# Performance work log

Measured on AMD Instinct MI355X. Metric: run time of the kernel, lower is better.

## Reference

```python
import jax, jax.numpy as jnp
import numpy as np

V = 50000   # input_size == output_size (one-hot vocab)
H = 256     # hidden_size
B = 512     # batch_size
L = 1       # num_layers

def setup_inputs() -> dict:
    key = jax.random.key(0)
    ks = jax.random.split(key, 9)
    s = 1.0 / np.sqrt(H)  # torch default uniform(-1/sqrt(H), 1/sqrt(H))
    inp = {
        "input": jax.random.randint(ks[0], (B,), 0, V, dtype=jnp.int64 if jax.config.jax_enable_x64 else jnp.int32),
        "target": jax.random.randint(ks[1], (B,), 0, V, dtype=jnp.int64 if jax.config.jax_enable_x64 else jnp.int32),
        "hidden": jax.random.normal(ks[2], (L, B, H), dtype=jnp.float32),
        "w_ih": jax.random.uniform(ks[3], (3 * H, V), jnp.float32, -s, s),
        "w_hh": jax.random.uniform(ks[4], (3 * H, H), jnp.float32, -s, s),
        "b_ih": jax.random.uniform(ks[5], (3 * H,), jnp.float32, -s, s),
        "b_hh": jax.random.uniform(ks[6], (3 * H,), jnp.float32, -s, s),
        "w_out": jax.random.uniform(ks[7], (V, H), jnp.float32, -s, s),
        "b_out": jax.random.uniform(ks[8], (V,), jnp.float32, -s, s),
    }
    return inp

def reference(input, target, hidden, w_ih, w_hh, b_ih, b_hh, w_out, b_out):
    # one-hot(input) @ w_ih.T is exactly a row-gather from w_ih.T  -> (B, 3H)
    h0 = hidden[0]                              # (B, H), num_layers == 1
    x_proj = w_ih.T[input] + b_ih               # (B, 3H)
    h_proj = h0 @ w_hh.T + b_hh                 # (B, 3H)
    xr, xz, xn = jnp.split(x_proj, 3, axis=-1)
    hr, hz, hn = jnp.split(h_proj, 3, axis=-1)
    r = jax.nn.sigmoid(xr + hr)                 # reset gate
    z = jax.nn.sigmoid(xz + hz)                 # update gate
    n = jnp.tanh(xn + r * hn)                   # candidate
    h1 = (1.0 - z) * n + z * h0                 # (B, H)
    logit = jnp.tanh(h1 @ w_out.T + b_out)      # (B, V)
    return logit, h1[None]                      # (B,V), (1,B,H)
```

## Files before the change

### kernel.cpp

```cpp
#include <hip/hip_runtime.h>
#include <hip/hip_bf16.h>

#define VOCAB 50000
#define HID   256
#define BATCH 512
#define GH    768

typedef __attribute__((ext_vector_type(8))) __bf16 bf16x8;
typedef __attribute__((ext_vector_type(4))) float f32x4;

union BFrag {
    bf16x8 v;
    uint4  q;
    unsigned short u[8];
};

__device__ __forceinline__ unsigned short f2bf(float f) {
    unsigned int x = __builtin_bit_cast(unsigned int, f);
    x += 0x7FFFu + ((x >> 16) & 1u);
    return (unsigned short)(x >> 16);
}

__device__ __forceinline__ float fast_sigmoid(float x) {
    return 1.0f / (1.0f + __expf(-x));
}
__device__ __forceinline__ float fast_tanh(float x) {
    return 1.0f - 2.0f / (1.0f + __expf(2.0f * x));
}

template <int EPI, int ASRC>
__global__ __launch_bounds__(256) void gemm_nt(
    const void* __restrict__ Asrc, const float* __restrict__ Bm,
    float* __restrict__ C, const float* __restrict__ bias,
    int Ncols, int mChunks)
{
    __shared__ char ldsA[64 * 512];

    const int tid  = threadIdx.x;
    const int wid  = tid >> 6;
    const int lane = tid & 63;
    const int r    = lane & 15;
    const int g    = lane >> 4;
    const int nbase = blockIdx.x * 64;
    const int col   = nbase + wid * 16 + r;
    const int bcol  = col < Ncols ? col : (Ncols - 1);

    BFrag bf[8];
    {
        const float4* wrow = reinterpret_cast<const float4*>(Bm + (size_t)bcol * 256);
        #pragma unroll
        for (int kk = 0; kk < 8; kk++) {
            float4 lo = wrow[kk * 8 + g * 2];
            float4 hi = wrow[kk * 8 + g * 2 + 1];
            bf[kk].u[0] = f2bf(lo.x); bf[kk].u[1] = f2bf(lo.y);
            bf[kk].u[2] = f2bf(lo.z); bf[kk].u[3] = f2bf(lo.w);
            bf[kk].u[4] = f2bf(hi.x); bf[kk].u[5] = f2bf(hi.y);
            bf[kk].u[6] = f2bf(hi.z); bf[kk].u[7] = f2bf(hi.w);
        }
    }
    float biasv = 0.0f;
    if (EPI == 1) biasv = bias[bcol];

    for (int c = 0; c < mChunks; c++) {
        const int mbase = (blockIdx.y * mChunks + c) * 64;

        if (ASRC == 1) {
            const uint4* src = reinterpret_cast<const uint4*>(
                (const unsigned short*)Asrc + (size_t)mbase * 256);
            #pragma unroll
            for (int i = 0; i < 8; i++) {
                int u   = tid + i * 256;
                int row = u >> 5, c16 = u & 31;
                uint4 vv = src[row * 32 + c16];
                int byte = (row * 512 + c16 * 16) ^ ((row & 7) << 4);
                *reinterpret_cast<uint4*>(&ldsA[byte]) = vv;
            }
        } else {
            const float4* src = reinterpret_cast<const float4*>(
                (const float*)Asrc + (size_t)mbase * 256);
            #pragma unroll
            for (int i = 0; i < 8; i++) {
                int u   = tid + i * 256;
                int row = u >> 5, c16 = u & 31;
                float4 lo = src[row * 64 + c16 * 2];
                float4 hi = src[row * 64 + c16 * 2 + 1];
                BFrag t;
                t.u[0] = f2bf(lo.x); t.u[1] = f2bf(lo.y);
                t.u[2] = f2bf(lo.z); t.u[3] = f2bf(lo.w);
                t.u[4] = f2bf(hi.x); t.u[5] = f2bf(hi.y);
                t.u[6] = f2bf(hi.z); t.u[7] = f2bf(hi.w);
                int byte = (row * 512 + c16 * 16) ^ ((row & 7) << 4);
                *reinterpret_cast<uint4*>(&ldsA[byte]) = t.q;
            }
        }
        __syncthreads();

        f32x4 acc[4];
        #pragma unroll
        for (int m = 0; m < 4; m++) acc[m] = (f32x4){0.f, 0.f, 0.f, 0.f};

        #pragma unroll
        for (int kk = 0; kk < 8; kk++) {
            #pragma unroll
            for (int m = 0; m < 4; m++) {
                int arow = m * 16 + r;
                int byte = (arow * 512 + kk * 64 + g * 16) ^ ((arow & 7) << 4);
                BFrag a;
                a.q = *reinterpret_cast<const uint4*>(&ldsA[byte]);
                acc[m] = __builtin_amdgcn_mfma_f32_16x16x32_bf16(a.v, bf[kk].v, acc[m], 0, 0, 0);
            }
        }

        if (col < Ncols) {
            #pragma unroll
            for (int m = 0; m < 4; m++) {
                #pragma unroll
                for (int j = 0; j < 4; j++) {
                    int row = mbase + m * 16 + g * 4 + j;
                    float v = acc[m][j];
                    if (EPI == 1) v = fast_tanh(v + biasv);
                    C[(size_t)row * Ncols + col] = v;
                }
            }
        }
        __syncthreads();
    }
}

__global__ __launch_bounds__(256) void gru_gate(
    const int* __restrict__ inp, const float* __restrict__ hidden,
    const float* __restrict__ w_ih, const float* __restrict__ b_ih,
    const float* __restrict__ b_hh, const float* __restrict__ hproj,
    float* __restrict__ h1out, unsigned short* __restrict__ h1bf)
{
    const int b = blockIdx.x;
    const int k = threadIdx.x;
    const int c = inp[b];

    float xr = w_ih[(size_t)k * VOCAB + c]         + b_ih[k];
    float xz = w_ih[(size_t)(k + 256) * VOCAB + c] + b_ih[k + 256];
    float xn = w_ih[(size_t)(k + 512) * VOCAB + c] + b_ih[k + 512];

    float hr = hproj[b * GH + k]       + b_hh[k];
    float hz = hproj[b * GH + 256 + k] + b_hh[k + 256];
    float hn = hproj[b * GH + 512 + k] + b_hh[k + 512];

    float rg = fast_sigmoid(xr + hr);
    float zg = fast_sigmoid(xz + hz);
    float ng = fast_tanh(xn + rg * hn);
    float h0 = hidden[b * HID + k];
    float h1 = (1.0f - zg) * ng + zg * h0;

    h1out[b * HID + k] = h1;
    h1bf[b * HID + k]  = f2bf(h1);
}

extern "C" void kernel_launch(void* const* d_in, const int* in_sizes, int n_in,
                              void* d_out, int out_size, void* d_ws, size_t ws_size,
                              hipStream_t stream) {
    const int*   input  = (const int*)  d_in[0];
    const float* hidden = (const float*)d_in[2];
    const float* w_ih   = (const float*)d_in[3];
    const float* w_hh   = (const float*)d_in[4];
    const float* b_ih   = (const float*)d_in[5];
    const float* b_hh   = (const float*)d_in[6];
    const float* w_out  = (const float*)d_in[7];
    const float* b_out  = (const float*)d_in[8];

    float* logit = (float*)d_out;
    float* h1    = (float*)d_out + (size_t)BATCH * VOCAB;

    float*          hproj = (float*)d_ws;
    unsigned short* h1bf  = (unsigned short*)((char*)d_ws + (size_t)BATCH * GH * 4);

    dim3 g1(GH / 64, BATCH / 64);
    gemm_nt<0, 0><<<g1, 256, 0, stream>>>(hidden, w_hh, hproj, nullptr, GH, 1);

    gru_gate<<<BATCH, 256, 0, stream>>>(input, hidden, w_ih, b_ih, b_hh, hproj, h1, h1bf);

    dim3 g3((VOCAB + 63) / 64, 1);
    gemm_nt<1, 1><<<g3, 256, 0, stream>>>(h1bf, w_out, logit, b_out, VOCAB, 8);
}
```

Baseline: 63.18 us.

## Drop LDS staging of A operand; load fragments directly from global with nontemporal access

The GEMM kernel no longer stages the A tile into shared memory behind barriers. Each wave now loads its MFMA A fragments directly from global memory, relying on L2/L1 because the bf16 h1 matrix is small and shared across all blocks. Weight loads for the large output projection and the logit stores use nontemporal hints to avoid polluting cache. The risk is that redundant global loads per wave, with 4x duplication across waves, add latency that LDS reuse previously hid.

```diff
diff --git a/kernel.cpp b/kernel.cpp
--- a/kernel.cpp
+++ b/kernel.cpp
@@ -8,10 +8,11 @@
 
 typedef __attribute__((ext_vector_type(8))) __bf16 bf16x8;
 typedef __attribute__((ext_vector_type(4))) float f32x4;
+typedef __attribute__((ext_vector_type(4))) unsigned int u32x4;
 
 union BFrag {
     bf16x8 v;
-    uint4  q;
+    u32x4  q;
     unsigned short u[8];
 };
 
@@ -28,34 +29,41 @@
     return 1.0f - 2.0f / (1.0f + __expf(2.0f * x));
 }
 
-template <int EPI, int ASRC>
+__device__ __forceinline__ void cvt8(BFrag& t, f32x4 lo, f32x4 hi) {
+    t.u[0] = f2bf(lo.x); t.u[1] = f2bf(lo.y);
+    t.u[2] = f2bf(lo.z); t.u[3] = f2bf(lo.w);
+    t.u[4] = f2bf(hi.x); t.u[5] = f2bf(hi.y);
+    t.u[6] = f2bf(hi.z); t.u[7] = f2bf(hi.w);
+}
+
+template <int EPI, int ASRC, int NTB>
 __global__ __launch_bounds__(256) void gemm_nt(
     const void* __restrict__ Asrc, const float* __restrict__ Bm,
     float* __restrict__ C, const float* __restrict__ bias,
     int Ncols, int mChunks)
 {
-    __shared__ char ldsA[64 * 512];
-
     const int tid  = threadIdx.x;
     const int wid  = tid >> 6;
     const int lane = tid & 63;
     const int r    = lane & 15;
     const int g    = lane >> 4;
-    const int nbase = blockIdx.x * 64;
-    const int col   = nbase + wid * 16 + r;
-    const int bcol  = col < Ncols ? col : (Ncols - 1);
+    const int col  = blockIdx.x * 64 + wid * 16 + r;
+    const int bcol = col < Ncols ? col : (Ncols - 1);
 
     BFrag bf[8];
     {
-        const float4* wrow = reinterpret_cast<const float4*>(Bm + (size_t)bcol * 256);
+        const f32x4* wrow = reinterpret_cast<const f32x4*>(Bm + (size_t)bcol * 256);
         #pragma unroll
         for (int kk = 0; kk < 8; kk++) {
-            float4 lo = wrow[kk * 8 + g * 2];
-            float4 hi = wrow[kk * 8 + g * 2 + 1];
-            bf[kk].u[0] = f2bf(lo.x); bf[kk].u[1] = f2bf(lo.y);
-            bf[kk].u[2] = f2bf(lo.z); bf[kk].u[3] = f2bf(lo.w);
-            bf[kk].u[4] = f2bf(hi.x); bf[kk].u[5] = f2bf(hi.y);
-            bf[kk].u[6] = f2bf(hi.z); bf[kk].u[7] = f2bf(hi.w);
+            f32x4 lo, hi;
+            if (NTB) {
+                lo = __builtin_nontemporal_load(&wrow[kk * 8 + g * 2]);
+                hi = __builtin_nontemporal_load(&wrow[kk * 8 + g * 2 + 1]);
+            } else {
+                lo = wrow[kk * 8 + g * 2];
+                hi = wrow[kk * 8 + g * 2 + 1];
+            }
+            cvt8(bf[kk], lo, hi);
         }
     }
     float biasv = 0.0f;
@@ -63,37 +71,6 @@
 
     for (int c = 0; c < mChunks; c++) {
         const int mbase = (blockIdx.y * mChunks + c) * 64;
-
-        if (ASRC == 1) {
-            const uint4* src = reinterpret_cast<const uint4*>(
-                (const unsigned short*)Asrc + (size_t)mbase * 256);
-            #pragma unroll
-            for (int i = 0; i < 8; i++) {
-                int u   = tid + i * 256;
-                int row = u >> 5, c16 = u & 31;
-                uint4 vv = src[row * 32 + c16];
-                int byte = (row * 512 + c16 * 16) ^ ((row & 7) << 4);
-                *reinterpret_cast<uint4*>(&ldsA[byte]) = vv;
-            }
-        } else {
-            const float4* src = reinterpret_cast<const float4*>(
-                (const float*)Asrc + (size_t)mbase * 256);
-            #pragma unroll
-            for (int i = 0; i < 8; i++) {
-                int u   = tid + i * 256;
-                int row = u >> 5, c16 = u & 31;
-                float4 lo = src[row * 64 + c16 * 2];
-                float4 hi = src[row * 64 + c16 * 2 + 1];
-                BFrag t;
-                t.u[0] = f2bf(lo.x); t.u[1] = f2bf(lo.y);
-                t.u[2] = f2bf(lo.z); t.u[3] = f2bf(lo.w);
-                t.u[4] = f2bf(hi.x); t.u[5] = f2bf(hi.y);
-                t.u[6] = f2bf(hi.z); t.u[7] = f2bf(hi.w);
-                int byte = (row * 512 + c16 * 16) ^ ((row & 7) << 4);
-                *reinterpret_cast<uint4*>(&ldsA[byte]) = t.q;
-            }
-        }
-        __syncthreads();
 
         f32x4 acc[4];
         #pragma unroll
@@ -103,10 +80,17 @@
         for (int kk = 0; kk < 8; kk++) {
             #pragma unroll
             for (int m = 0; m < 4; m++) {
-                int arow = m * 16 + r;
-                int byte = (arow * 512 + kk * 64 + g * 16) ^ ((arow & 7) << 4);
+                const int arow = mbase + m * 16 + r;
                 BFrag a;
-                a.q = *reinterpret_cast<const uint4*>(&ldsA[byte]);
+                if (ASRC == 1) {
+                    const u32x4* ap = reinterpret_cast<const u32x4*>(
+                        (const unsigned short*)Asrc + (size_t)arow * 256);
+                    a.q = ap[kk * 4 + g];
+                } else {
+                    const f32x4* ap = reinterpret_cast<const f32x4*>(
+                        (const float*)Asrc + (size_t)arow * 256);
+                    cvt8(a, ap[kk * 8 + g * 2], ap[kk * 8 + g * 2 + 1]);
+                }
                 acc[m] = __builtin_amdgcn_mfma_f32_16x16x32_bf16(a.v, bf[kk].v, acc[m], 0, 0, 0);
             }
         }
@@ -118,12 +102,15 @@
                 for (int j = 0; j < 4; j++) {
                     int row = mbase + m * 16 + g * 4 + j;
                     float v = acc[m][j];
-                    if (EPI == 1) v = fast_tanh(v + biasv);
-                    C[(size_t)row * Ncols + col] = v;
+                    if (EPI == 1) {
+                        v = fast_tanh(v + biasv);
+                        __builtin_nontemporal_store(v, &C[(size_t)row * Ncols + col]);
+                    } else {
+                        C[(size_t)row * Ncols + col] = v;
+                    }
                 }
             }
         }
-        __syncthreads();
     }
 }
 
@@ -174,10 +161,10 @@
     unsigned short* h1bf  = (unsigned short*)((char*)d_ws + (size_t)BATCH * GH * 4);
 
     dim3 g1(GH / 64, BATCH / 64);
-    gemm_nt<0, 0><<<g1, 256, 0, stream>>>(hidden, w_hh, hproj, nullptr, GH, 1);
+    gemm_nt<0, 0, 0><<<g1, 256, 0, stream>>>(hidden, w_hh, hproj, nullptr, GH, 1);
 
     gru_gate<<<BATCH, 256, 0, stream>>>(input, hidden, w_ih, b_ih, b_hh, hproj, h1, h1bf);
 
     dim3 g3((VOCAB + 63) / 64, 1);
-    gemm_nt<1, 1><<<g3, 256, 0, stream>>>(h1bf, w_out, logit, b_out, VOCAB, 8);
+    gemm_nt<1, 1, 1><<<g3, 256, 0, stream>>>(h1bf, w_out, logit, b_out, VOCAB, 8);
 }
```

Measured after the change: 154.2 us. 2.44x slower.

## Double-buffer A chunks in LDS and overlap loads with MFMA compute

Applied to the files above, without the earlier changes.

The GEMM kernel now keeps two LDS buffers. It prefetches the next 64-row A chunk into registers while computing the current chunk, and delays the C store of the previous chunk so it overlaps with the next load and compute. The goal is to hide global load and store latency behind MFMA work in the large output GEMM, which loops over 8 chunks. In exchange, the kernel doubles LDS use and keeps more registers live (staging registers plus two accumulator sets), which may lower occupancy.

```diff
diff --git a/kernel.cpp b/kernel.cpp
--- a/kernel.cpp
+++ b/kernel.cpp
@@ -8,10 +8,11 @@
 
 typedef __attribute__((ext_vector_type(8))) __bf16 bf16x8;
 typedef __attribute__((ext_vector_type(4))) float f32x4;
+typedef __attribute__((ext_vector_type(4))) unsigned int u32x4;
 
 union BFrag {
     bf16x8 v;
-    uint4  q;
+    u32x4  q;
     unsigned short u[8];
 };
 
@@ -28,77 +29,70 @@
     return 1.0f - 2.0f / (1.0f + __expf(2.0f * x));
 }
 
+__device__ __forceinline__ void cvt8(BFrag& t, f32x4 lo, f32x4 hi) {
+    t.u[0] = f2bf(lo.x); t.u[1] = f2bf(lo.y);
+    t.u[2] = f2bf(lo.z); t.u[3] = f2bf(lo.w);
+    t.u[4] = f2bf(hi.x); t.u[5] = f2bf(hi.y);
+    t.u[6] = f2bf(hi.z); t.u[7] = f2bf(hi.w);
+}
+
 template <int EPI, int ASRC>
 __global__ __launch_bounds__(256) void gemm_nt(
     const void* __restrict__ Asrc, const float* __restrict__ Bm,
     float* __restrict__ C, const float* __restrict__ bias,
     int Ncols, int mChunks)
 {
-    __shared__ char ldsA[64 * 512];
+    __shared__ char ldsA[2][64 * 512];
 
     const int tid  = threadIdx.x;
     const int wid  = tid >> 6;
     const int lane = tid & 63;
     const int r    = lane & 15;
     const int g    = lane >> 4;
-    const int nbase = blockIdx.x * 64;
-    const int col   = nbase + wid * 16 + r;
-    const int bcol  = col < Ncols ? col : (Ncols - 1);
+    const int col  = blockIdx.x * 64 + wid * 16 + r;
+    const int bcol = col < Ncols ? col : (Ncols - 1);
 
     BFrag bf[8];
     {
-        const float4* wrow = reinterpret_cast<const float4*>(Bm + (size_t)bcol * 256);
+        const f32x4* wrow = reinterpret_cast<const f32x4*>(Bm + (size_t)bcol * 256);
         #pragma unroll
-        for (int kk = 0; kk < 8; kk++) {
-            float4 lo = wrow[kk * 8 + g * 2];
-            float4 hi = wrow[kk * 8 + g * 2 + 1];
-            bf[kk].u[0] = f2bf(lo.x); bf[kk].u[1] = f2bf(lo.y);
-            bf[kk].u[2] = f2bf(lo.z); bf[kk].u[3] = f2bf(lo.w);
-            bf[kk].u[4] = f2bf(hi.x); bf[kk].u[5] = f2bf(hi.y);
-            bf[kk].u[6] = f2bf(hi.z); bf[kk].u[7] = f2bf(hi.w);
-        }
+        for (int kk = 0; kk < 8; kk++)
+            cvt8(bf[kk], wrow[kk * 8 + g * 2], wrow[kk * 8 + g * 2 + 1]);
     }
     float biasv = 0.0f;
     if (EPI == 1) biasv = bias[bcol];
 
-    for (int c = 0; c < mChunks; c++) {
+    u32x4 streg[8];
+    auto load_chunk = [&](int c) {
         const int mbase = (blockIdx.y * mChunks + c) * 64;
-
         if (ASRC == 1) {
-            const uint4* src = reinterpret_cast<const uint4*>(
+            const u32x4* src = reinterpret_cast<const u32x4*>(
                 (const unsigned short*)Asrc + (size_t)mbase * 256);
             #pragma unroll
-            for (int i = 0; i < 8; i++) {
-                int u   = tid + i * 256;
-                int row = u >> 5, c16 = u & 31;
-                uint4 vv = src[row * 32 + c16];
-                int byte = (row * 512 + c16 * 16) ^ ((row & 7) << 4);
-                *reinterpret_cast<uint4*>(&ldsA[byte]) = vv;
-            }
+            for (int i = 0; i < 8; i++) streg[i] = src[tid + i * 256];
         } else {
-            const float4* src = reinterpret_cast<const float4*>(
+            const f32x4* src = reinterpret_cast<const f32x4*>(
                 (const float*)Asrc + (size_t)mbase * 256);
             #pragma unroll
             for (int i = 0; i < 8; i++) {
-                int u   = tid + i * 256;
-                int row = u >> 5, c16 = u & 31;
-                float4 lo = src[row * 64 + c16 * 2];
-                float4 hi = src[row * 64 + c16 * 2 + 1];
-                BFrag t;
-                t.u[0] = f2bf(lo.x); t.u[1] = f2bf(lo.y);
-                t.u[2] = f2bf(lo.z); t.u[3] = f2bf(lo.w);
-                t.u[4] = f2bf(hi.x); t.u[5] = f2bf(hi.y);
-                t.u[6] = f2bf(hi.z); t.u[7] = f2bf(hi.w);
-                int byte = (row * 512 + c16 * 16) ^ ((row & 7) << 4);
-                *reinterpret_cast<uint4*>(&ldsA[byte]) = t.q;
+                int u = tid + i * 256;
+                BFrag t; cvt8(t, src[2 * u], src[2 * u + 1]);
+                streg[i] = t.q;
             }
         }
-        __syncthreads();
-
-        f32x4 acc[4];
+    };
+    auto write_lds = [&](int buf) {
+        #pragma unroll
+        for (int i = 0; i < 8; i++) {
+            int u = tid + i * 256;
+            int row = u >> 5, c16 = u & 31;
+            int byte = (row * 512 + c16 * 16) ^ ((row & 7) << 4);
+            *reinterpret_cast<u32x4*>(&ldsA[buf][byte]) = streg[i];
+        }
+    };
+    auto compute = [&](int buf, f32x4 (&acc)[4]) {
         #pragma unroll
         for (int m = 0; m < 4; m++) acc[m] = (f32x4){0.f, 0.f, 0.f, 0.f};
-
         #pragma unroll
         for (int kk = 0; kk < 8; kk++) {
             #pragma unroll
@@ -106,25 +100,46 @@
                 int arow = m * 16 + r;
                 int byte = (arow * 512 + kk * 64 + g * 16) ^ ((arow & 7) << 4);
                 BFrag a;
-                a.q = *reinterpret_cast<const uint4*>(&ldsA[byte]);
+                a.q = *reinterpret_cast<const u32x4*>(&ldsA[buf][byte]);
                 acc[m] = __builtin_amdgcn_mfma_f32_16x16x32_bf16(a.v, bf[kk].v, acc[m], 0, 0, 0);
             }
         }
-
-        if (col < Ncols) {
+    };
+    auto store_c = [&](int c, f32x4 (&acc)[4]) {
+        if (col >= Ncols) return;
+        const int mbase = (blockIdx.y * mChunks + c) * 64;
+        #pragma unroll
+        for (int m = 0; m < 4; m++) {
             #pragma unroll
-            for (int m = 0; m < 4; m++) {
-                #pragma unroll
-                for (int j = 0; j < 4; j++) {
-                    int row = mbase + m * 16 + g * 4 + j;
-                    float v = acc[m][j];
-                    if (EPI == 1) v = fast_tanh(v + biasv);
-                    C[(size_t)row * Ncols + col] = v;
-                }
+            for (int j = 0; j < 4; j++) {
+                int row = mbase + m * 16 + g * 4 + j;
+                float v = acc[m][j];
+                if (EPI == 1) v = fast_tanh(v + biasv);
+                C[(size_t)row * Ncols + col] = v;
             }
         }
+    };
+
+    f32x4 accA[4], accB[4];
+    load_chunk(0);
+
+    for (int c = 0; c < mChunks; c += 2) {
+        write_lds(c & 1);
         __syncthreads();
+        if (c > 0) store_c(c - 1, accB);
+        if (c + 1 < mChunks) load_chunk(c + 1);
+        compute(c & 1, accA);
+
+        if (c + 1 < mChunks) {
+            write_lds((c + 1) & 1);
+            __syncthreads();
+            store_c(c, accA);
+            if (c + 2 < mChunks) load_chunk(c + 2);
+            compute((c + 1) & 1, accB);
+        }
     }
+    if (mChunks & 1) store_c(mChunks - 1, accA);
+    else             store_c(mChunks - 1, accB);
 }
 
 __global__ __launch_bounds__(256) void gru_gate(
```

Measured after the change: 65.91 us. 4.3% more time.

## Split output GEMM over batch tiles in the grid instead of looping per block

Applied to the files above, without the earlier changes.

Each output GEMM block previously loaded a 64-column slice of W_out into registers once and looped over all eight 64-row batch chunks. Now the grid is batch-tile by column-tile with one 64x64 tile per block, and batch is the fastest-varying grid index so neighbouring blocks reuse the same W_out columns through cache. The aim is to replace roughly three looping blocks per CU with many independent blocks, plus a launch-bounds occupancy hint, so the memory-bound output writes overlap better. The cost is that each W_out slice is fetched and converted to bf16 eight times instead of once, which depends on cache hits to stay cheap.

```diff
diff --git a/kernel.cpp b/kernel.cpp
--- a/kernel.cpp
+++ b/kernel.cpp
@@ -8,10 +8,11 @@
 
 typedef __attribute__((ext_vector_type(8))) __bf16 bf16x8;
 typedef __attribute__((ext_vector_type(4))) float f32x4;
+typedef __attribute__((ext_vector_type(4))) unsigned int u32x4;
 
 union BFrag {
     bf16x8 v;
-    uint4  q;
+    u32x4  q;
     unsigned short u[8];
 };
 
@@ -28,11 +29,17 @@
     return 1.0f - 2.0f / (1.0f + __expf(2.0f * x));
 }
 
+__device__ __forceinline__ void cvt8(BFrag& t, f32x4 lo, f32x4 hi) {
+    t.u[0] = f2bf(lo.x); t.u[1] = f2bf(lo.y);
+    t.u[2] = f2bf(lo.z); t.u[3] = f2bf(lo.w);
+    t.u[4] = f2bf(hi.x); t.u[5] = f2bf(hi.y);
+    t.u[6] = f2bf(hi.z); t.u[7] = f2bf(hi.w);
+}
+
 template <int EPI, int ASRC>
-__global__ __launch_bounds__(256) void gemm_nt(
+__global__ __launch_bounds__(256, 4) void gemm_tile(
     const void* __restrict__ Asrc, const float* __restrict__ Bm,
-    float* __restrict__ C, const float* __restrict__ bias,
-    int Ncols, int mChunks)
+    float* __restrict__ C, const float* __restrict__ bias, int Ncols)
 {
     __shared__ char ldsA[64 * 512];
 
@@ -41,89 +48,72 @@
     const int lane = tid & 63;
     const int r    = lane & 15;
     const int g    = lane >> 4;
-    const int nbase = blockIdx.x * 64;
-    const int col   = nbase + wid * 16 + r;
+    const int mbase = blockIdx.x * 64;
+    const int col   = blockIdx.y * 64 + wid * 16 + r;
     const int bcol  = col < Ncols ? col : (Ncols - 1);
 
     BFrag bf[8];
     {
-        const float4* wrow = reinterpret_cast<const float4*>(Bm + (size_t)bcol * 256);
+        const f32x4* wrow = reinterpret_cast<const f32x4*>(Bm + (size_t)bcol * 256);
         #pragma unroll
-        for (int kk = 0; kk < 8; kk++) {
-            float4 lo = wrow[kk * 8 + g * 2];
-            float4 hi = wrow[kk * 8 + g * 2 + 1];
-            bf[kk].u[0] = f2bf(lo.x); bf[kk].u[1] = f2bf(lo.y);
-            bf[kk].u[2] = f2bf(lo.z); bf[kk].u[3] = f2bf(lo.w);
-            bf[kk].u[4] = f2bf(hi.x); bf[kk].u[5] = f2bf(hi.y);
-            bf[kk].u[6] = f2bf(hi.z); bf[kk].u[7] = f2bf(hi.w);
-        }
+        for (int kk = 0; kk < 8; kk++)
+            cvt8(bf[kk], wrow[kk * 8 + g * 2], wrow[kk * 8 + g * 2 + 1]);
     }
     float biasv = 0.0f;
     if (EPI == 1) biasv = bias[bcol];
 
-    for (int c = 0; c < mChunks; c++) {
-        const int mbase = (blockIdx.y * mChunks + c) * 64;
+    if (ASRC == 1) {
+        const u32x4* src = reinterpret_cast<const u32x4*>(
+            (const unsigned short*)Asrc + (size_t)mbase * 256);
+        #pragma unroll
+        for (int i = 0; i < 8; i++) {
+            int u = tid + i * 256;
+            int row = u >> 5, c16 = u & 31;
+            u32x4 vv = src[u];
+            int byte = (row * 512 + c16 * 16) ^ ((row & 7) << 4);
+            *reinterpret_cast<u32x4*>(&ldsA[byte]) = vv;
+        }
+    } else {
+        const f32x4* src = reinterpret_cast<const f32x4*>(
+            (const float*)Asrc + (size_t)mbase * 256);
+        #pragma unroll
+        for (int i = 0; i < 8; i++) {
+            int u = tid + i * 256;
+            int row = u >> 5, c16 = u & 31;
+            BFrag t; cvt8(t, src[2 * u], src[2 * u + 1]);
+            int byte = (row * 512 + c16 * 16) ^ ((row & 7) << 4);
+            *reinterpret_cast<u32x4*>(&ldsA[byte]) = t.q;
+        }
+    }
+    __syncthreads();
 
-        if (ASRC == 1) {
-            const uint4* src = reinterpret_cast<const uint4*>(
-                (const unsigned short*)Asrc + (size_t)mbase * 256);
+    f32x4 acc[4];
+    #pragma unroll
+    for (int m = 0; m < 4; m++) acc[m] = (f32x4){0.f, 0.f, 0.f, 0.f};
+
+    #pragma unroll
+    for (int kk = 0; kk < 8; kk++) {
+        #pragma unroll
+        for (int m = 0; m < 4; m++) {
+            int arow = m * 16 + r;
+            int byte = (arow * 512 + kk * 64 + g * 16) ^ ((arow & 7) << 4);
+            BFrag a;
+            a.q = *reinterpret_cast<const u32x4*>(&ldsA[byte]);
+            acc[m] = __builtin_amdgcn_mfma_f32_16x16x32_bf16(a.v, bf[kk].v, acc[m], 0, 0, 0);
+        }
+    }
+
+    if (col < Ncols) {
+        #pragma unroll
+        for (int m = 0; m < 4; m++) {
             #pragma unroll
-            for (int i = 0; i < 8; i++) {
-                int u   = tid + i * 256;
-                int row = u >> 5, c16 = u & 31;
-                uint4 vv = src[row * 32 + c16];
-                int byte = (row * 512 + c16 * 16) ^ ((row & 7) << 4);
-                *reinterpret_cast<uint4*>(&ldsA[byte]) = vv;
-            }
-        } else {
-            const float4* src = reinterpret_cast<const float4*>(
-                (const float*)Asrc + (size_t)mbase * 256);
-            #pragma unroll
-            for (int i = 0; i < 8; i++) {
-                int u   = tid + i * 256;
-                int row = u >> 5, c16 = u & 31;
-                float4 lo = src[row * 64 + c16 * 2];
-                float4 hi = src[row * 64 + c16 * 2 + 1];
-                BFrag t;
-                t.u[0] = f2bf(lo.x); t.u[1] = f2bf(lo.y);
-                t.u[2] = f2bf(lo.z); t.u[3] = f2bf(lo.w);
-                t.u[4] = f2bf(hi.x); t.u[5] = f2bf(hi.y);
-                t.u[6] = f2bf(hi.z); t.u[7] = f2bf(hi.w);
-                int byte = (row * 512 + c16 * 16) ^ ((row & 7) << 4);
-                *reinterpret_cast<uint4*>(&ldsA[byte]) = t.q;
+            for (int j = 0; j < 4; j++) {
+                int row = mbase + m * 16 + g * 4 + j;
+                float v = acc[m][j];
+                if (EPI == 1) v = fast_tanh(v + biasv);
+                C[(size_t)row * Ncols + col] = v;
             }
         }
-        __syncthreads();
-
-        f32x4 acc[4];
-        #pragma unroll
-        for (int m = 0; m < 4; m++) acc[m] = (f32x4){0.f, 0.f, 0.f, 0.f};
-
-        #pragma unroll
-        for (int kk = 0; kk < 8; kk++) {
-            #pragma unroll
-            for (int m = 0; m < 4; m++) {
-                int arow = m * 16 + r;
-                int byte = (arow * 512 + kk * 64 + g * 16) ^ ((arow & 7) << 4);
-                BFrag a;
-                a.q = *reinterpret_cast<const uint4*>(&ldsA[byte]);
-                acc[m] = __builtin_amdgcn_mfma_f32_16x16x32_bf16(a.v, bf[kk].v, acc[m], 0, 0, 0);
-            }
-        }
-
-        if (col < Ncols) {
-            #pragma unroll
-            for (int m = 0; m < 4; m++) {
-                #pragma unroll
-                for (int j = 0; j < 4; j++) {
-                    int row = mbase + m * 16 + g * 4 + j;
-                    float v = acc[m][j];
-                    if (EPI == 1) v = fast_tanh(v + biasv);
-                    C[(size_t)row * Ncols + col] = v;
-                }
-            }
-        }
-        __syncthreads();
     }
 }
 
@@ -173,11 +163,12 @@
     float*          hproj = (float*)d_ws;
     unsigned short* h1bf  = (unsigned short*)((char*)d_ws + (size_t)BATCH * GH * 4);
 
-    dim3 g1(GH / 64, BATCH / 64);
-    gemm_nt<0, 0><<<g1, 256, 0, stream>>>(hidden, w_hh, hproj, nullptr, GH, 1);
+    dim3 g1(BATCH / 64, GH / 64);
+    gemm_tile<0, 0><<<g1, 256, 0, stream>>>(hidden, w_hh, hproj, nullptr, GH);
 
-    gru_gate<<<BATCH, 256, 0, stream>>>(input, hidden, w_ih, b_ih, b_hh, hproj, h1, h1bf);
+    gru_gate<<<BATCH, 256, 0, stream>>>(input, hidden, w_ih, b_ih, b_hh, hproj,
+                                        h1, h1bf);
 
-    dim3 g3((VOCAB + 63) / 64, 1);
-    gemm_nt<1, 1><<<g3, 256, 0, stream>>>(h1bf, w_out, logit, b_out, VOCAB, 8);
+    dim3 g3(BATCH / 64, (VOCAB + 63) / 64);
+    gemm_tile<1, 1><<<g3, 256, 0, stream>>>(h1bf, w_out, logit, b_out, VOCAB);
 }
```

Result: slower. 90.36 us (+43.0%).
